# Kernel tuning notes

Hardware: AMD Instinct MI355X
Metric: run time of the kernel (lower is better)

The kernel has to match this reference:

```python
import jax, jax.numpy as jnp
import numpy as np

B, C, H, W = 32, 192, 32, 32
CH, STRIDE = 8, 2
FEAT = CH * (H // STRIDE) * (W // STRIDE)  # 8*16*16 = 2048


def setup_inputs() -> dict:
    key = jax.random.key(0)
    ks = jax.random.split(key, 7)
    inp = jax.random.normal(ks[0], (B, C, H, W), jnp.float32)
    w_left_out = jax.random.normal(ks[1], (B, C, H, W), jnp.float32)
    conv_w = jax.random.normal(ks[2], (CH, C, 3, 3), jnp.float32) * 0.05
    conv_b = jnp.zeros((CH,), jnp.float32)
    # small scale keeps diag(U) moderate so exp(s) stays finite
    lin_w = jax.random.normal(ks[3], (C * C, FEAT), jnp.float32) * 0.01
    lin_b = jax.random.normal(ks[4], (C * C,), jnp.float32) * 0.1
    s_sign = jnp.sign(jax.random.normal(ks[5], (C,), jnp.float32))
    return dict(inp=inp, w_left_out=w_left_out, conv_w=conv_w, conv_b=conv_b,
                lin_w=lin_w, lin_b=lin_b, s_sign=s_sign)


def _cond_net(x, conv_w, conv_b, lin_w, lin_b):
    # Conv2d(C->CH, k=3, stride=2, pad=1) + ReLU + Flatten + Linear(FEAT -> C*C)
    h = jax.lax.conv_general_dilated(
        x, conv_w, window_strides=(STRIDE, STRIDE), padding=((1, 1), (1, 1)),
        dimension_numbers=('NCHW', 'OIHW', 'NCHW'))
    h = jax.nn.relu(h + conv_b[None, :, None, None])
    return h.reshape(x.shape[0], -1) @ lin_w.T + lin_b  # [B, C*C]


def reference(inp, w_left_out, conv_w, conv_b, lin_w, lin_b, s_sign):
    b, c, height, width = inp.shape
    cond = _cond_net(w_left_out, conv_w, conv_b, lin_w, lin_b)
    mats = cond.reshape(b, c, c)
    # batched LU: a = p @ l @ u (scipy convention, unit-diag l)
    p, l, u = jax.vmap(jax.scipy.linalg.lu)(mats)
    s = jnp.diagonal(u, axis1=1, axis2=2)          # [B, C] raw diag(U)
    eye = jnp.eye(c, dtype=inp.dtype)
    l_full = jnp.tril(l, -1) + eye                  # l * l_mask + I
    u_full = jnp.triu(u, 1) + (s_sign[None, :] * jnp.exp(s))[..., None] * eye
    weight = p @ l_full @ u_full                    # [B, C, C]
    # batched 1x1 conv == per-sample GEMM over spatial positions
    out = jnp.einsum('bij,bjhw->bihw', weight, inp)
    log_w = jnp.mean(jnp.sum(s, axis=1))            # sum(w_s) averaged over batch
    log_det = (height * width) * log_w
    return out, log_det
```

## Files before the change

kernel.cpp:

```cpp
#include <hip/hip_runtime.h>
#include <math.h>


#define NFEAT 2048
#define NN    36864

__global__ __launch_bounds__(256) void conv_kernel(const float* __restrict__ w,
                                                   const float* __restrict__ cw,
                                                   float* __restrict__ hpart) {
  int blk = blockIdx.x;
  int b = blk >> 2, cs = blk & 3;
  int tid = threadIdx.x;
  int oy = tid >> 4, ox = tid & 15;
  __shared__ float wlds[8 * 48 * 9];
  for (int idx = tid; idx < 8 * 48 * 9; idx += 256) {
    int ch = idx / 432, rem = idx - ch * 432;
    int c = rem / 9, kk = rem - c * 9;
    wlds[idx] = cw[ch * 1728 + (cs * 48 + c) * 9 + kk];
  }
  __syncthreads();
  float acc[8];
#pragma unroll
  for (int ch = 0; ch < 8; ++ch) acc[ch] = 0.f;
  const float* img0 = w + (((size_t)b * 192 + cs * 48) << 10);
  for (int c = 0; c < 48; ++c) {
    const float* img = img0 + ((size_t)c << 10);
    float iv[9];
#pragma unroll
    for (int ky = 0; ky < 3; ++ky)
#pragma unroll
      for (int kx = 0; kx < 3; ++kx) {
        int iy = 2 * oy - 1 + ky, ix = 2 * ox - 1 + kx;
        bool ok = (iy >= 0) & (iy < 32) & (ix >= 0) & (ix < 32);
        iv[ky * 3 + kx] = ok ? img[iy * 32 + ix] : 0.f;
      }
#pragma unroll
    for (int ch = 0; ch < 8; ++ch) {
      const float* wp = &wlds[(ch * 48 + c) * 9];
      float s = acc[ch];
#pragma unroll
      for (int t = 0; t < 9; ++t) s = fmaf(iv[t], wp[t], s);
      acc[ch] = s;
    }
  }
  size_t base = ((size_t)(cs * 32 + b) << 11) + tid;
#pragma unroll
  for (int ch = 0; ch < 8; ++ch) hpart[base + (ch << 8)] = acc[ch];
}

__global__ __launch_bounds__(256) void hreduce_kernel(const float* __restrict__ hpart,
                                                      const float* __restrict__ cb,
                                                      float* __restrict__ h_t) {
  int g = blockIdx.x * 256 + threadIdx.x;
  int k = g & 2047, b = g >> 11;
  float s = 0.f;
#pragma unroll
  for (int cs = 0; cs < 4; ++cs) s += hpart[(((size_t)(cs * 32 + b)) << 11) + k];
  s += cb[k >> 8];
  s = fmaxf(s, 0.f);
  h_t[((size_t)k << 5) + b] = s;
}

__global__ __launch_bounds__(256) void linear_kernel(const float* __restrict__ h_t,
                                                     const float* __restrict__ lw,
                                                     const float* __restrict__ lb,
                                                     float* __restrict__ mats) {
  __shared__ float Wbuf[64 * 68];
  __shared__ float Hbuf[64 * 36];
  int tid = threadIdx.x;
  int n0 = blockIdx.x << 6;
  int half = tid >> 5;
  int bb = tid & 31;
  int nb = half << 3;
  float accq0[8], accq1[8], accq2[8], accq3[8];
#pragma unroll
  for (int j = 0; j < 8; ++j) { accq0[j] = 0.f; accq1[j] = 0.f; accq2[j] = 0.f; accq3[j] = 0.f; }

#define LIN_CHUNK(ACC)                                                         \
  {                                                                            \
    int koff = kc << 6;                                                        \
    _Pragma("unroll") for (int j = 0; j < 4; ++j) {                            \
      int f = tid + (j << 8);                                                  \
      int row = f >> 4, c4 = (f & 15) << 2;                                    \
      *(float4*)(Wbuf + row * 68 + c4) =                                       \
          *(const float4*)(lw + (size_t)(n0 + row) * 2048 + koff + c4);        \
    }                                                                          \
    _Pragma("unroll") for (int j = 0; j < 2; ++j) {                            \
      int f = tid + (j << 8);                                                  \
      int kr = f >> 3, b4 = (f & 7) << 2;                                      \
      *(float4*)(Hbuf + kr * 36 + b4) =                                        \
          *(const float4*)(h_t + (((size_t)(koff + kr)) << 5) + b4);           \
    }                                                                          \
    __syncthreads();                                                           \
    _Pragma("unroll 4") for (int k4 = 0; k4 < 16; ++k4) {                      \
      int kk = k4 << 2;                                                        \
      float h0 = Hbuf[(kk + 0) * 36 + bb];                                     \
      float h1 = Hbuf[(kk + 1) * 36 + bb];                                     \
      float h2 = Hbuf[(kk + 2) * 36 + bb];                                     \
      float h3 = Hbuf[(kk + 3) * 36 + bb];                                     \
      _Pragma("unroll") for (int j = 0; j < 8; ++j) {                          \
        float4 w4 = *(const float4*)(Wbuf + (nb + j) * 68 + kk);               \
        float s = ACC[j];                                                      \
        s = fmaf(w4.x, h0, s);                                                 \
        s = fmaf(w4.y, h1, s);                                                 \
        s = fmaf(w4.z, h2, s);                                                 \
        s = fmaf(w4.w, h3, s);                                                 \
        ACC[j] = s;                                                            \
      }                                                                        \
    }                                                                          \
    __syncthreads();                                                           \
  }

  for (int kc = 0; kc < 8; ++kc)  LIN_CHUNK(accq0)
  for (int kc = 8; kc < 16; ++kc) LIN_CHUNK(accq1)
  for (int kc = 16; kc < 24; ++kc) LIN_CHUNK(accq2)
  for (int kc = 24; kc < 32; ++kc) LIN_CHUNK(accq3)
#undef LIN_CHUNK

  float o[8];
#pragma unroll
  for (int j = 0; j < 8; ++j)
    o[j] = ((accq0[j] + accq1[j]) + accq2[j]) + accq3[j] + lb[n0 + nb + j];
  float* mp = mats + (size_t)bb * NN + n0 + nb;
  *(float4*)(mp + 0) = make_float4(o[0], o[1], o[2], o[3]);
  *(float4*)(mp + 4) = make_float4(o[4], o[5], o[6], o[7]);
}

#define CAT_(A, B) A##B
#define CAT(A, B) CAT_(A, B)
#define PR_0(R) CAT(pA, R).x
#define PR_1(R) CAT(pA, R).y
#define PR_2(R) CAT(pA, R).z
#define PR_3(R) CAT(pA, R).w
#define PR_4(R) CAT(pB, R).x
#define PR_5(R) CAT(pB, R).y
#define PR_6(R) CAT(pB, R).z
#define PR_7(R) CAT(pB, R).w
#define PR(R, K) CAT(PR_, K)(R)
#define UU_0 uA.x
#define UU_1 uA.y
#define UU_2 uA.z
#define UU_3 uA.w
#define UU_4 uB.x
#define UU_5 uB.y
#define UU_6 uB.z
#define UU_7 uB.w
#define UU(K) CAT(UU_, K)
#define UPDJ(R, J) PR(R, J) = fmaf(-m, UU(J), PR(R, J));
#define TAIL_0(R) UPDJ(R,1) UPDJ(R,2) UPDJ(R,3) UPDJ(R,4) UPDJ(R,5) UPDJ(R,6) UPDJ(R,7)
#define TAIL_1(R) UPDJ(R,2) UPDJ(R,3) UPDJ(R,4) UPDJ(R,5) UPDJ(R,6) UPDJ(R,7)
#define TAIL_2(R) UPDJ(R,3) UPDJ(R,4) UPDJ(R,5) UPDJ(R,6) UPDJ(R,7)
#define TAIL_3(R) UPDJ(R,4) UPDJ(R,5) UPDJ(R,6) UPDJ(R,7)
#define TAIL_4(R) UPDJ(R,5) UPDJ(R,6) UPDJ(R,7)
#define TAIL_5(R) UPDJ(R,6) UPDJ(R,7)
#define TAIL_6(R) UPDJ(R,7)
#define TAIL_7(R)
#define UPDROW(R, KK, kg)                                                      \
  if (CAT(lg, R) > (kg)) {                                                     \
    float m = PR(R, KK) * recip;                                               \
    PR(R, KK) = m;                                                             \
    CAT(TAIL_, KK)(R)                                                          \
  }
#define PSTEP(KK) {                                                            \
  const int kg = kp + KK;                                                      \
  float bv = -1.f; int br = 0x7fffffff;                                        \
  { float v = fabsf(PR(0,KK)); if (lg0 >= kg && (v > bv || (v == bv && lg0 < br))) { bv = v; br = lg0; } } \
  { float v = fabsf(PR(1,KK)); if (lg1 >= kg && (v > bv || (v == bv && lg1 < br))) { bv = v; br = lg1; } } \
  { float v = fabsf(PR(2,KK)); if (lg2 >= kg && (v > bv || (v == bv && lg2 < br))) { bv = v; br = lg2; } } \
  for (int msk = 1; msk <= 32; msk <<= 1) {                                    \
    float ov = __shfl_xor(bv, msk, 64);                                        \
    int obr = __shfl_xor(br, msk, 64);                                         \
    if (ov > bv || (ov == bv && obr < br)) { bv = ov; br = obr; }              \
  }                                                                            \
  bool own0 = (lg0 == br), own1 = (lg1 == br), own2 = (lg2 == br);             \
  float4 sA = own1 ? pA1 : (own2 ? pA2 : pA0);                                 \
  float4 sB = own1 ? pB1 : (own2 ? pB2 : pB0);                                 \
  int owner = (int)__ffsll(__ballot(own0 | own1 | own2)) - 1;                  \
  float4 uA, uB;                                                               \
  uA.x = __shfl(sA.x, owner); uA.y = __shfl(sA.y, owner);                      \
  uA.z = __shfl(sA.z, owner); uA.w = __shfl(sA.w, owner);                      \
  uB.x = __shfl(sB.x, owner); uB.y = __shfl(sB.y, owner);                      \
  uB.z = __shfl(sB.z, owner); uB.w = __shfl(sB.w, owner);                      \
  float piv = UU(KK);                                                          \
  float recip = 1.0f / piv;                                                    \
  if (tid == 0) {                                                              \
    diagU[kg] = piv;                                                           \
    int t0 = rowmap[kg], t1 = rowmap[br];                                      \
    rowmap[kg] = t1; rowmap[br] = t0;                                          \
  }                                                                            \
  lg0 = (lg0 == kg) ? br : ((lg0 == br) ? kg : lg0);                           \
  lg1 = (lg1 == kg) ? br : ((lg1 == br) ? kg : lg1);                           \
  lg2 = (lg2 == kg) ? br : ((lg2 == br) ? kg : lg2);                           \
  UPDROW(0, KK, kg)                                                            \
  UPDROW(1, KK, kg)                                                            \
  UPDROW(2, KK, kg)                                                            \
}
#define FMA4(D, M, S) {                                                        \
  float mm = (M);                                                              \
  D.x = fmaf(-mm, S.x, D.x); D.y = fmaf(-mm, S.y, D.y);                        \
  D.z = fmaf(-mm, S.z, D.z); D.w = fmaf(-mm, S.w, D.w);                        \
}

__global__ __launch_bounds__(768, 1) void lu_kernel(float* __restrict__ A0,
                                                    const float* __restrict__ ssign,
                                                    float* __restrict__ ssum) {
  __shared__ float4 As4[192 * 49];
  __shared__ int rowmap[192];
  __shared__ float diagU[192];
  __shared__ float4 dval4[48];
  float* As = (float*)As4;
  float* dvalf = (float*)dval4;
  (void)As;
  int b = blockIdx.x;
  int tid = threadIdx.x;
  float* __restrict__ A = A0 + (size_t)b * NN;

#pragma unroll
  for (int j = 0; j < 12; ++j) {
    int chunk = tid + 768 * j;
    int row = chunk / 48, q = chunk - row * 48;
    As4[row * 49 + q] = *(const float4*)(A + row * 192 + 4 * q);
  }
  for (int i = tid; i < 192; i += 768) rowmap[i] = i;
  __syncthreads();

  int lg0 = tid, lg1 = tid + 64, lg2 = tid + 128;

  for (int p = 0; p < 24; ++p) {
    const int kp = p << 3;
    const int pc = kp >> 2;
    if (tid < 64) {
      float4 pA0 = As4[tid * 49 + pc],         pB0 = As4[tid * 49 + pc + 1];
      float4 pA1 = As4[(tid + 64) * 49 + pc],  pB1 = As4[(tid + 64) * 49 + pc + 1];
      float4 pA2 = As4[(tid + 128) * 49 + pc], pB2 = As4[(tid + 128) * 49 + pc + 1];
      PSTEP(0) PSTEP(1) PSTEP(2) PSTEP(3) PSTEP(4) PSTEP(5) PSTEP(6) PSTEP(7)
      As4[tid * 49 + pc] = pA0;         As4[tid * 49 + pc + 1] = pB0;
      As4[(tid + 64) * 49 + pc] = pA1;  As4[(tid + 64) * 49 + pc + 1] = pB1;
      As4[(tid + 128) * 49 + pc] = pA2; As4[(tid + 128) * 49 + pc + 1] = pB2;
    }
    __syncthreads();
    {
      const int qp1 = (kp + 8) >> 2;
      const int q = tid >> 4;
      const int slot = tid & 15;
      if (q >= qp1) {
        const int ur0 = rowmap[kp + 0], ur1 = rowmap[kp + 1];
        const int ur2 = rowmap[kp + 2], ur3 = rowmap[kp + 3];
        const int ur4 = rowmap[kp + 4], ur5 = rowmap[kp + 5];
        const int ur6 = rowmap[kp + 6], ur7 = rowmap[kp + 7];
        float4 u40 = As4[ur0 * 49 + q], u41 = As4[ur1 * 49 + q];
        float4 u42 = As4[ur2 * 49 + q], u43 = As4[ur3 * 49 + q];
        float4 u44 = As4[ur4 * 49 + q], u45 = As4[ur5 * 49 + q];
        float4 u46 = As4[ur6 * 49 + q], u47 = As4[ur7 * 49 + q];
        { float4 la = As4[ur1 * 49 + pc];
          FMA4(u41, la.x, u40) }
        { float4 la = As4[ur2 * 49 + pc];
          FMA4(u42, la.x, u40) FMA4(u42, la.y, u41) }
        { float4 la = As4[ur3 * 49 + pc];
          FMA4(u43, la.x, u40) FMA4(u43, la.y, u41) FMA4(u43, la.z, u42) }
        { float4 la = As4[ur4 * 49 + pc];
          FMA4(u44, la.x, u40) FMA4(u44, la.y, u41) FMA4(u44, la.z, u42) FMA4(u44, la.w, u43) }
        { float4 la = As4[ur5 * 49 + pc]; float4 lb = As4[ur5 * 49 + pc + 1];
          FMA4(u45, la.x, u40) FMA4(u45, la.y, u41) FMA4(u45, la.z, u42) FMA4(u45, la.w, u43)
          FMA4(u45, lb.x, u44) }
        { float4 la = As4[ur6 * 49 + pc]; float4 lb = As4[ur6 * 49 + pc + 1];
          FMA4(u46, la.x, u40) FMA4(u46, la.y, u41) FMA4(u46, la.z, u42) FMA4(u46, la.w, u43)
          FMA4(u46, lb.x, u44) FMA4(u46, lb.y, u45) }
        { float4 la = As4[ur7 * 49 + pc]; float4 lb = As4[ur7 * 49 + pc + 1];
          FMA4(u47, la.x, u40) FMA4(u47, la.y, u41) FMA4(u47, la.z, u42) FMA4(u47, la.w, u43)
          FMA4(u47, lb.x, u44) FMA4(u47, lb.y, u45) FMA4(u47, lb.z, u46) }
        for (int i = 0; i < 12; ++i) {
          int s = slot + (i << 4);
          if (s >= kp + 8) {
            int phys = rowmap[s];
            float4 la = As4[phys * 49 + pc];
            float4 lb = As4[phys * 49 + pc + 1];
            float4 c = As4[phys * 49 + q];
            FMA4(c, la.x, u40) FMA4(c, la.y, u41) FMA4(c, la.z, u42) FMA4(c, la.w, u43)
            FMA4(c, lb.x, u44) FMA4(c, lb.y, u45) FMA4(c, lb.z, u46) FMA4(c, lb.w, u47)
            As4[phys * 49 + q] = c;
          }
        }
      }
    }
    __syncthreads();
  }

  if (tid == 0) {
    float s = 0.f;
    for (int i = 0; i < 192; ++i) s += diagU[i];
    ssum[b] = s;
  }
  if (tid < 192) dvalf[tid] = ssign[tid] * expf(diagU[tid]) - diagU[tid];
  __syncthreads();
  {
    const int r = tid >> 2;
    const int tq = tid & 3;
    int i = r;
    int phys = rowmap[r];
    float di = dvalf[i];
    float* __restrict__ G = A + (size_t)phys * 192;
    int qi = i >> 2;
    for (int j = 0; j < 12; ++j) {
      int q = tq + 4 * j;
      if (q > qi) continue;
      float4 g4 = *(float4*)(G + 4 * q);
      float4 a4 = As4[phys * 49 + q];
      float4 d4 = dval4[q];
      if (q == qi) {
        int c0 = 4 * q;
        g4.x = (c0 + 0 < i) ? g4.x + a4.x * d4.x : ((c0 + 0 == i) ? g4.x + di : g4.x);
        g4.y = (c0 + 1 < i) ? g4.y + a4.y * d4.y : ((c0 + 1 == i) ? g4.y + di : g4.y);
        g4.z = (c0 + 2 < i) ? g4.z + a4.z * d4.z : ((c0 + 2 == i) ? g4.z + di : g4.z);
        g4.w = (c0 + 3 < i) ? g4.w + a4.w * d4.w : ((c0 + 3 == i) ? g4.w + di : g4.w);
      } else {
        g4.x += a4.x * d4.x;
        g4.y += a4.y * d4.y;
        g4.z += a4.z * d4.z;
        g4.w += a4.w * d4.w;
      }
      *(float4*)(G + 4 * q) = g4;
    }
  }
}

__global__ __launch_bounds__(256) void out_kernel(const float* __restrict__ wt,
                                                  const float* __restrict__ inp,
                                                  const float* __restrict__ ssum,
                                                  float* __restrict__ out) {
  int blk = blockIdx.x;
  int b = blk / 24, rem = blk % 24;
  int it = rem >> 3, jt = rem & 7;
  int i0 = it << 6, hw0 = jt << 7;
  int tid = threadIdx.x;
  int tx = tid & 31, ty = tid >> 5;
  __shared__ float wlds[64 * 36];
  __shared__ float xlds[32 * 128];
  const float* wb = wt + (size_t)b * NN;
  const float* xb = inp + (((size_t)b * 192) << 10);
  float acc[8][4];
#pragma unroll
  for (int r = 0; r < 8; ++r)
#pragma unroll
    for (int c = 0; c < 4; ++c) acc[r][c] = 0.f;
  for (int kc = 0; kc < 6; ++kc) {
    __syncthreads();
#pragma unroll
    for (int j = 0; j < 2; ++j) {
      int f4 = tid + (j << 8);
      int row = f4 >> 3, c4 = (f4 & 7) << 2;
      float4 v = *(const float4*)(wb + (size_t)(i0 + row) * 192 + (kc << 5) + c4);
      *(float4*)(wlds + row * 36 + c4) = v;
    }
#pragma unroll
    for (int j = 0; j < 4; ++j) {
      int f4 = tid + (j << 8);
      int row = f4 >> 5, c4 = (f4 & 31) << 2;
      float4 v = *(const float4*)(xb + (((size_t)(kc << 5) + row) << 10) + hw0 + c4);
      *(float4*)(xlds + (row << 7) + c4) = v;
    }
    __syncthreads();
#pragma unroll 4
    for (int k = 0; k < 32; ++k) {
      float4 xv = *(const float4*)(xlds + (k << 7) + (tx << 2));
      float wr[8];
#pragma unroll
      for (int r = 0; r < 8; ++r) wr[r] = wlds[(ty * 8 + r) * 36 + k];
#pragma unroll
      for (int r = 0; r < 8; ++r) {
        acc[r][0] = fmaf(wr[r], xv.x, acc[r][0]);
        acc[r][1] = fmaf(wr[r], xv.y, acc[r][1]);
        acc[r][2] = fmaf(wr[r], xv.z, acc[r][2]);
        acc[r][3] = fmaf(wr[r], xv.w, acc[r][3]);
      }
    }
  }
  float* ob = out + (((size_t)b * 192 + i0 + ty * 8) << 10) + hw0 + (tx << 2);
#pragma unroll
  for (int r = 0; r < 8; ++r) {
    float4 v = make_float4(acc[r][0], acc[r][1], acc[r][2], acc[r][3]);
    *(float4*)(ob + ((size_t)r << 10)) = v;
  }
  if (blk == 0 && tid == 0) {
    float s = 0.f;
    for (int i = 0; i < 32; ++i) s += ssum[i];
    out[6291456] = 32.f * s;
  }
}

extern "C" void kernel_launch(void* const* d_in, const int* in_sizes, int n_in,
                              void* d_out, int out_size, void* d_ws, size_t ws_size,
                              hipStream_t stream) {
  const float* inp = (const float*)d_in[0];
  const float* wlo = (const float*)d_in[1];
  const float* cw  = (const float*)d_in[2];
  const float* cb  = (const float*)d_in[3];
  const float* lw  = (const float*)d_in[4];
  const float* lb  = (const float*)d_in[5];
  const float* ss  = (const float*)d_in[6];
  float* out = (float*)d_out;
  float* ws = (float*)d_ws;
  float* hpart = ws;
  float* h_t   = ws + 262144;
  float* mats  = ws + 327680;
  float* ssum  = ws + 1507328;
  hipLaunchKernelGGL(conv_kernel,    dim3(128), dim3(256), 0, stream, wlo, cw, hpart);
  hipLaunchKernelGGL(hreduce_kernel, dim3(256), dim3(256), 0, stream, hpart, cb, h_t);
  hipLaunchKernelGGL(linear_kernel,  dim3(576), dim3(256), 0, stream, h_t, lw, lb, mats);
  hipLaunchKernelGGL(lu_kernel,      dim3(32),  dim3(768), 0, stream, mats, ss, ssum);
  hipLaunchKernelGGL(out_kernel,     dim3(768), dim3(256), 0, stream, mats, inp, ssum, out);
}
```

Baseline: 489.5 us.

## Overlap next panel factorization with trailing update via lookahead in LU kernel

Restructures the blocked LU loop with a one-panel lookahead. Each iteration first finishes the U-row triangular solve and updates the next panel's two columns. Wave 0 then factors the next panel while the other waves update the remaining trailing columns, taking the serial panel step off the critical path. Rowmap entries are snapshotted before the panel swaps rows, at the cost of extra barriers per iteration and repeated U-row loads.

```diff
diff --git a/kernel.cpp b/kernel.cpp
--- a/kernel.cpp
+++ b/kernel.cpp
@@ -162,7 +162,7 @@
     CAT(TAIL_, KK)(R)                                                          \
   }
 #define PSTEP(KK) {                                                            \
-  const int kg = kp + KK;                                                      \
+  const int kg = kpP + KK;                                                     \
   float bv = -1.f; int br = 0x7fffffff;                                        \
   { float v = fabsf(PR(0,KK)); if (lg0 >= kg && (v > bv || (v == bv && lg0 < br))) { bv = v; br = lg0; } } \
   { float v = fabsf(PR(1,KK)); if (lg1 >= kg && (v > bv || (v == bv && lg1 < br))) { bv = v; br = lg1; } } \
@@ -200,6 +200,17 @@
   D.x = fmaf(-mm, S.x, D.x); D.y = fmaf(-mm, S.y, D.y);                        \
   D.z = fmaf(-mm, S.z, D.z); D.w = fmaf(-mm, S.w, D.w);                        \
 }
+#define PANEL(KPV) {                                                           \
+  const int kpP = (KPV);                                                       \
+  const int pcP = kpP >> 2;                                                    \
+  float4 pA0 = As4[tid * 49 + pcP],         pB0 = As4[tid * 49 + pcP + 1];     \
+  float4 pA1 = As4[(tid + 64) * 49 + pcP],  pB1 = As4[(tid + 64) * 49 + pcP + 1]; \
+  float4 pA2 = As4[(tid + 128) * 49 + pcP], pB2 = As4[(tid + 128) * 49 + pcP + 1]; \
+  PSTEP(0) PSTEP(1) PSTEP(2) PSTEP(3) PSTEP(4) PSTEP(5) PSTEP(6) PSTEP(7)     \
+  As4[tid * 49 + pcP] = pA0;         As4[tid * 49 + pcP + 1] = pB0;            \
+  As4[(tid + 64) * 49 + pcP] = pA1;  As4[(tid + 64) * 49 + pcP + 1] = pB1;     \
+  As4[(tid + 128) * 49 + pcP] = pA2; As4[(tid + 128) * 49 + pcP + 1] = pB2;    \
+}
 
 __global__ __launch_bounds__(768, 1) void lu_kernel(float* __restrict__ A0,
                                                     const float* __restrict__ ssign,
@@ -208,9 +219,7 @@
   __shared__ int rowmap[192];
   __shared__ float diagU[192];
   __shared__ float4 dval4[48];
-  float* As = (float*)As4;
   float* dvalf = (float*)dval4;
-  (void)As;
   int b = blockIdx.x;
   int tid = threadIdx.x;
   float* __restrict__ A = A0 + (size_t)b * NN;
@@ -226,62 +235,107 @@
 
   int lg0 = tid, lg1 = tid + 64, lg2 = tid + 128;
 
-  for (int p = 0; p < 24; ++p) {
+  if (tid < 64) { PANEL(0) }
+  __syncthreads();
+
+  const int qg = tid >> 4;
+  const int slot = tid & 15;
+
+  for (int p = 0; p < 23; ++p) {
     const int kp = p << 3;
     const int pc = kp >> 2;
+    const int qp1 = pc + 2;
+
+    if (tid >= qp1 && tid < 48) {
+      const int q = tid;
+      const int ur0 = rowmap[kp + 0], ur1 = rowmap[kp + 1];
+      const int ur2 = rowmap[kp + 2], ur3 = rowmap[kp + 3];
+      const int ur4 = rowmap[kp + 4], ur5 = rowmap[kp + 5];
+      const int ur6 = rowmap[kp + 6], ur7 = rowmap[kp + 7];
+      float4 u40 = As4[ur0 * 49 + q], u41 = As4[ur1 * 49 + q];
+      float4 u42 = As4[ur2 * 49 + q], u43 = As4[ur3 * 49 + q];
+      float4 u44 = As4[ur4 * 49 + q], u45 = As4[ur5 * 49 + q];
+      float4 u46 = As4[ur6 * 49 + q], u47 = As4[ur7 * 49 + q];
+      { float4 la = As4[ur1 * 49 + pc];
+        FMA4(u41, la.x, u40) }
+      { float4 la = As4[ur2 * 49 + pc];
+        FMA4(u42, la.x, u40) FMA4(u42, la.y, u41) }
+      { float4 la = As4[ur3 * 49 + pc];
+        FMA4(u43, la.x, u40) FMA4(u43, la.y, u41) FMA4(u43, la.z, u42) }
+      { float4 la = As4[ur4 * 49 + pc];
+        FMA4(u44, la.x, u40) FMA4(u44, la.y, u41) FMA4(u44, la.z, u42) FMA4(u44, la.w, u43) }
+      { float4 la = As4[ur5 * 49 + pc]; float4 lb2 = As4[ur5 * 49 + pc + 1];
+        FMA4(u45, la.x, u40) FMA4(u45, la.y, u41) FMA4(u45, la.z, u42) FMA4(u45, la.w, u43)
+        FMA4(u45, lb2.x, u44) }
+      { float4 la = As4[ur6 * 49 + pc]; float4 lb2 = As4[ur6 * 49 + pc + 1];
+        FMA4(u46, la.x, u40) FMA4(u46, la.y, u41) FMA4(u46, la.z, u42) FMA4(u46, la.w, u43)
+        FMA4(u46, lb2.x, u44) FMA4(u46, lb2.y, u45) }
+      { float4 la = As4[ur7 * 49 + pc]; float4 lb2 = As4[ur7 * 49 + pc + 1];
+        FMA4(u47, la.x, u40) FMA4(u47, la.y, u41) FMA4(u47, la.z, u42) FMA4(u47, la.w, u43)
+        FMA4(u47, lb2.x, u44) FMA4(u47, lb2.y, u45) FMA4(u47, lb2.z, u46) }
+      As4[ur0 * 49 + q] = u40; As4[ur1 * 49 + q] = u41;
+      As4[ur2 * 49 + q] = u42; As4[ur3 * 49 + q] = u43;
+      As4[ur4 * 49 + q] = u44; As4[ur5 * 49 + q] = u45;
+      As4[ur6 * 49 + q] = u46; As4[ur7 * 49 + q] = u47;
+    }
+    __syncthreads();
+
+    {
+      const int col = qp1 + (tid >= 384 ? 1 : 0);
+      const int rsl = tid - (tid >= 384 ? 384 : 0);
+      const int s = kp + 8 + rsl;
+      if (s < 192) {
+        const int ua0 = rowmap[kp + 0], ua1 = rowmap[kp + 1];
+        const int ua2 = rowmap[kp + 2], ua3 = rowmap[kp + 3];
+        const int ua4 = rowmap[kp + 4], ua5 = rowmap[kp + 5];
+        const int ua6 = rowmap[kp + 6], ua7 = rowmap[kp + 7];
+        float4 u40 = As4[ua0 * 49 + col], u41 = As4[ua1 * 49 + col];
+        float4 u42 = As4[ua2 * 49 + col], u43 = As4[ua3 * 49 + col];
+        float4 u44 = As4[ua4 * 49 + col], u45 = As4[ua5 * 49 + col];
+        float4 u46 = As4[ua6 * 49 + col], u47 = As4[ua7 * 49 + col];
+        int phys = rowmap[s];
+        float4 la = As4[phys * 49 + pc];
+        float4 lb2 = As4[phys * 49 + pc + 1];
+        float4 c = As4[phys * 49 + col];
+        FMA4(c, la.x, u40) FMA4(c, la.y, u41) FMA4(c, la.z, u42) FMA4(c, la.w, u43)
+        FMA4(c, lb2.x, u44) FMA4(c, lb2.y, u45) FMA4(c, lb2.z, u46) FMA4(c, lb2.w, u47)
+        As4[phys * 49 + col] = c;
+      }
+    }
+    int php0, php1, php2, php3, php4, php5, php6, php7, php8, php9, php10, php11;
+#define SNAP(I) CAT(php, I) = rowmap[slot + (I << 4)];
+    SNAP(0) SNAP(1) SNAP(2) SNAP(3) SNAP(4) SNAP(5) SNAP(6)
+    SNAP(7) SNAP(8) SNAP(9) SNAP(10) SNAP(11)
+#undef SNAP
+    __syncthreads();
+
     if (tid < 64) {
-      float4 pA0 = As4[tid * 49 + pc],         pB0 = As4[tid * 49 + pc + 1];
-      float4 pA1 = As4[(tid + 64) * 49 + pc],  pB1 = As4[(tid + 64) * 49 + pc + 1];
-      float4 pA2 = As4[(tid + 128) * 49 + pc], pB2 = As4[(tid + 128) * 49 + pc + 1];
-      PSTEP(0) PSTEP(1) PSTEP(2) PSTEP(3) PSTEP(4) PSTEP(5) PSTEP(6) PSTEP(7)
-      As4[tid * 49 + pc] = pA0;         As4[tid * 49 + pc + 1] = pB0;
-      As4[(tid + 64) * 49 + pc] = pA1;  As4[(tid + 64) * 49 + pc + 1] = pB1;
-      As4[(tid + 128) * 49 + pc] = pA2; As4[(tid + 128) * 49 + pc + 1] = pB2;
-    }
-    __syncthreads();
-    {
-      const int qp1 = (kp + 8) >> 2;
-      const int q = tid >> 4;
-      const int slot = tid & 15;
-      if (q >= qp1) {
-        const int ur0 = rowmap[kp + 0], ur1 = rowmap[kp + 1];
-        const int ur2 = rowmap[kp + 2], ur3 = rowmap[kp + 3];
-        const int ur4 = rowmap[kp + 4], ur5 = rowmap[kp + 5];
-        const int ur6 = rowmap[kp + 6], ur7 = rowmap[kp + 7];
-        float4 u40 = As4[ur0 * 49 + q], u41 = As4[ur1 * 49 + q];
-        float4 u42 = As4[ur2 * 49 + q], u43 = As4[ur3 * 49 + q];
-        float4 u44 = As4[ur4 * 49 + q], u45 = As4[ur5 * 49 + q];
-        float4 u46 = As4[ur6 * 49 + q], u47 = As4[ur7 * 49 + q];
-        { float4 la = As4[ur1 * 49 + pc];
-          FMA4(u41, la.x, u40) }
-        { float4 la = As4[ur2 * 49 + pc];
-          FMA4(u42, la.x, u40) FMA4(u42, la.y, u41) }
-        { float4 la = As4[ur3 * 49 + pc];
-          FMA4(u43, la.x, u40) FMA4(u43, la.y, u41) FMA4(u43, la.z, u42) }
-        { float4 la = As4[ur4 * 49 + pc];
-          FMA4(u44, la.x, u40) FMA4(u44, la.y, u41) FMA4(u44, la.z, u42) FMA4(u44, la.w, u43) }
-        { float4 la = As4[ur5 * 49 + pc]; float4 lb = As4[ur5 * 49 + pc + 1];
-          FMA4(u45, la.x, u40) FMA4(u45, la.y, u41) FMA4(u45, la.z, u42) FMA4(u45, la.w, u43)
-          FMA4(u45, lb.x, u44) }
-        { float4 la = As4[ur6 * 49 + pc]; float4 lb = As4[ur6 * 49 + pc + 1];
-          FMA4(u46, la.x, u40) FMA4(u46, la.y, u41) FMA4(u46, la.z, u42) FMA4(u46, la.w, u43)
-          FMA4(u46, lb.x, u44) FMA4(u46, lb.y, u45) }
-        { float4 la = As4[ur7 * 49 + pc]; float4 lb = As4[ur7 * 49 + pc + 1];
-          FMA4(u47, la.x, u40) FMA4(u47, la.y, u41) FMA4(u47, la.z, u42) FMA4(u47, la.w, u43)
-          FMA4(u47, lb.x, u44) FMA4(u47, lb.y, u45) FMA4(u47, lb.z, u46) }
-        for (int i = 0; i < 12; ++i) {
-          int s = slot + (i << 4);
-          if (s >= kp + 8) {
-            int phys = rowmap[s];
-            float4 la = As4[phys * 49 + pc];
-            float4 lb = As4[phys * 49 + pc + 1];
-            float4 c = As4[phys * 49 + q];
-            FMA4(c, la.x, u40) FMA4(c, la.y, u41) FMA4(c, la.z, u42) FMA4(c, la.w, u43)
-            FMA4(c, lb.x, u44) FMA4(c, lb.y, u45) FMA4(c, lb.z, u46) FMA4(c, lb.w, u47)
-            As4[phys * 49 + q] = c;
-          }
-        }
-      }
+      PANEL(kp + 8)
+    } else if (qg >= qp1 + 2) {
+      const int q = qg;
+      const int ub0 = rowmap[kp + 0], ub1 = rowmap[kp + 1];
+      const int ub2 = rowmap[kp + 2], ub3 = rowmap[kp + 3];
+      const int ub4 = rowmap[kp + 4], ub5 = rowmap[kp + 5];
+      const int ub6 = rowmap[kp + 6], ub7 = rowmap[kp + 7];
+      float4 u40 = As4[ub0 * 49 + q], u41 = As4[ub1 * 49 + q];
+      float4 u42 = As4[ub2 * 49 + q], u43 = As4[ub3 * 49 + q];
+      float4 u44 = As4[ub4 * 49 + q], u45 = As4[ub5 * 49 + q];
+      float4 u46 = As4[ub6 * 49 + q], u47 = As4[ub7 * 49 + q];
+#define GEMMROW(I) {                                                           \
+      int s = slot + (I << 4);                                                 \
+      if (s >= kp + 8) {                                                       \
+        int phys = CAT(php, I);                                                \
+        float4 la = As4[phys * 49 + pc];                                       \
+        float4 lb2 = As4[phys * 49 + pc + 1];                                  \
+        float4 c = As4[phys * 49 + q];                                         \
+        FMA4(c, la.x, u40) FMA4(c, la.y, u41) FMA4(c, la.z, u42) FMA4(c, la.w, u43) \
+        FMA4(c, lb2.x, u44) FMA4(c, lb2.y, u45) FMA4(c, lb2.z, u46) FMA4(c, lb2.w, u47) \
+        As4[phys * 49 + q] = c;                                                \
+      }                                                                        \
+    }
+      GEMMROW(0) GEMMROW(1) GEMMROW(2) GEMMROW(3) GEMMROW(4) GEMMROW(5)
+      GEMMROW(6) GEMMROW(7) GEMMROW(8) GEMMROW(9) GEMMROW(10) GEMMROW(11)
+#undef GEMMROW
     }
     __syncthreads();
   }
```

New measurement: 476.7 us. -2.6%, faster.
